# Kernel tuning notes

Measured on AMD Instinct MI355X. Metric: run time of the kernel, lower is better.

Reference implementation:

```python
import jax, jax.numpy as jnp
import numpy as np

D_MODEL = 1024
N_HEAD = 16
D_K = D_MODEL // N_HEAD


def setup_inputs() -> dict:
    key = jax.random.key(0)
    ks = jax.random.split(key, 11)
    B, S = 4, 2048
    s = 1.0 / np.sqrt(D_MODEL)
    return {
        "q": jax.random.normal(ks[0], (B, S, D_MODEL), jnp.float32),
        "k": jax.random.normal(ks[1], (B, S, D_MODEL), jnp.float32),
        "v": jax.random.normal(ks[2], (B, S, D_MODEL), jnp.float32),
        "w_q": jax.random.normal(ks[3], (D_MODEL, D_MODEL), jnp.float32) * s,
        "b_q": jnp.zeros((D_MODEL,), jnp.float32),
        "w_k": jax.random.normal(ks[4], (D_MODEL, D_MODEL), jnp.float32) * s,
        "b_k": jnp.zeros((D_MODEL,), jnp.float32),
        "w_v": jax.random.normal(ks[5], (D_MODEL, D_MODEL), jnp.float32) * s,
        "b_v": jnp.zeros((D_MODEL,), jnp.float32),
        "w_o": jax.random.normal(ks[6], (D_MODEL, D_MODEL), jnp.float32) * s,
        "b_o": jnp.zeros((D_MODEL,), jnp.float32),
    }


def reference(q, k, v, w_q, b_q, w_k, b_k, w_v, b_v, w_o, b_o):
    B, S, _ = q.shape
    # projections (torch Linear: x @ W^T + b)
    qp = q @ w_q.T + b_q
    kp = k @ w_k.T + b_k
    vp = v @ w_v.T + b_v
    # split heads -> [B, H, S, d_k]
    qh = qp.reshape(B, S, N_HEAD, D_K).transpose(0, 2, 1, 3)
    kh = kp.reshape(B, S, N_HEAD, D_K).transpose(0, 2, 1, 3)
    vh = vp.reshape(B, S, N_HEAD, D_K).transpose(0, 2, 1, 3)
    # scaled dot-product attention
    scores = jnp.einsum("bhqd,bhkd->bhqk", qh, kh) / jnp.sqrt(jnp.float32(D_K)).astype(qh.dtype)
    attn = jax.nn.softmax(scores, axis=-1)
    out = jnp.einsum("bhqk,bhkd->bhqd", attn, vh)
    # merge heads -> [B, S, d_model]
    out = out.transpose(0, 2, 1, 3).reshape(B, S, D_MODEL)
    return out @ w_o.T + b_o
```

## Files before the change

kernel.cpp:

```cpp
#include <hip/hip_runtime.h>
#include <hip/hip_bf16.h>
#include <stdint.h>

#define D_MODEL 1024
#define SEQ     2048
#define NBATCH  4
#define NHEAD   16
#define MROWS   (NBATCH*SEQ)

typedef __attribute__((ext_vector_type(8))) short short8;
typedef __attribute__((ext_vector_type(4))) float floatx4;
typedef __attribute__((ext_vector_type(2))) unsigned int uint2v;

#if __has_builtin(__builtin_amdgcn_exp2f)
#define EXP2(x) __builtin_amdgcn_exp2f(x)
#else
#define EXP2(x) exp2f(x)
#endif

__device__ __forceinline__ unsigned short f2bf(float f) {
  unsigned int x;
  __builtin_memcpy(&x, &f, 4);
  x += 0x7fffu + ((x >> 16) & 1u);
  return (unsigned short)(x >> 16);
}

__device__ __forceinline__ unsigned int pk2(float a, float b) {
  __hip_bfloat162 h = __float22bfloat162_rn(make_float2(a, b));
  unsigned int u;
  __builtin_memcpy(&u, &h, 4);
  return u;
}

__device__ __forceinline__ void gl_lds16(const unsigned short* g, unsigned short* l) {
  __builtin_amdgcn_global_load_lds(
      (const __attribute__((address_space(1))) unsigned int*)g,
      (__attribute__((address_space(3))) unsigned int*)l, 16, 0, 0);
}

__global__ __launch_bounds__(256)
void cvt_all(const float* __restrict__ q, const float* __restrict__ k,
             const float* __restrict__ v, const float* __restrict__ wq,
             const float* __restrict__ wk, const float* __restrict__ wv,
             const float* __restrict__ wo,
             unsigned short* __restrict__ dq, unsigned short* __restrict__ dk,
             unsigned short* __restrict__ dv, unsigned short* __restrict__ dwq,
             unsigned short* __restrict__ dwk, unsigned short* __restrict__ dwv,
             unsigned short* __restrict__ dwo) {
  const unsigned QV4 = (MROWS * D_MODEL) / 4u;
  const unsigned WV4 = (D_MODEL * D_MODEL) / 4u;
  const unsigned total = 3u * QV4 + 4u * WV4;
  for (unsigned i = blockIdx.x * 256u + threadIdx.x; i < total;
       i += gridDim.x * 256u) {
    const float* s;
    unsigned short* d;
    unsigned off;
    if (i < 3u * QV4) {
      const unsigned t = i >> 21;
      off = i & (QV4 - 1u);
      s = (t == 0) ? q : (t == 1) ? k : v;
      d = (t == 0) ? dq : (t == 1) ? dk : dv;
    } else {
      const unsigned j = i - 3u * QV4;
      const unsigned t = j >> 18;
      off = j & (WV4 - 1u);
      s = (t == 0) ? wq : (t == 1) ? wk : (t == 2) ? wv : wo;
      d = (t == 0) ? dwq : (t == 1) ? dwk : (t == 2) ? dwv : dwo;
    }
    const floatx4 f = *(const floatx4*)(s + (size_t)off * 4);
    uint2v u;
    u.x = pk2(f[0], f[1]);
    u.y = pk2(f[2], f[3]);
    *(uint2v*)(d + (size_t)off * 4) = u;
  }
}

template <bool OUT_F32>
__global__ __launch_bounds__(256)
void gemm_bt_bias(const unsigned short* __restrict__ A,
                  const unsigned short* __restrict__ W,
                  const float* __restrict__ bias, void* __restrict__ Y_,
                  int M, int N, int K, float scale) {
  __shared__ __attribute__((aligned(16))) unsigned short As[2][128 * 32];
  __shared__ __attribute__((aligned(16))) unsigned short Bs[2][128 * 32];
  const int tid  = threadIdx.x;
  const int lane = tid & 63;
  const int w    = tid >> 6;
  const int rho  = lane & 15;
  const int quad = lane >> 4;
  const int ntile = N >> 7;
  const int cpx = gridDim.x >> 3;
  const int wg  = (blockIdx.x & 7) * cpx + (blockIdx.x >> 3);
  const int bx = wg % ntile;
  const int by = wg / ntile;
  const int tm = by << 7, tn = bx << 7;
  const int wrow = (w >> 1) << 6;
  const int wcol = (w & 1) << 6;

  const int srow = lane >> 2;
  const int scol = (lane & 3) << 3;
  const unsigned short* gA = A + (size_t)(tm + w * 32 + srow) * K + scol;
  const unsigned short* gB = W + (size_t)(tn + w * 32 + srow) * K + scol;
  unsigned short* lA0 = &As[0][(w * 32) * 32];
  unsigned short* lA1 = &As[1][(w * 32) * 32];
  unsigned short* lB0 = &Bs[0][(w * 32) * 32];
  unsigned short* lB1 = &Bs[1][(w * 32) * 32];

  floatx4 acc[4][4] = {};

  gl_lds16(gA, lA0);
  gl_lds16(gA + 16 * (size_t)K, lA0 + 16 * 32);
  gl_lds16(gB, lB0);
  gl_lds16(gB + 16 * (size_t)K, lB0 + 16 * 32);
  __syncthreads();

  for (int kk = 0; kk < K; kk += 32) {
    const int cur = (kk >> 5) & 1;
    if (kk + 32 < K) {
      unsigned short* dA = cur ? lA0 : lA1;
      unsigned short* dB = cur ? lB0 : lB1;
      gl_lds16(gA + kk + 32, dA);
      gl_lds16(gA + 16 * (size_t)K + kk + 32, dA + 16 * 32);
      gl_lds16(gB + kk + 32, dB);
      gl_lds16(gB + 16 * (size_t)K + kk + 32, dB + 16 * 32);
    }
    const unsigned short* as = &As[cur][0];
    const unsigned short* bs = &Bs[cur][0];
    short8 af[4], bfr[4];
#pragma unroll
    for (int i = 0; i < 4; i++) {
      af[i]  = *(const short8*)&as[(wrow + i * 16 + rho) * 32 + quad * 8];
      bfr[i] = *(const short8*)&bs[(wcol + i * 16 + rho) * 32 + quad * 8];
    }
#pragma unroll
    for (int i = 0; i < 4; i++)
#pragma unroll
      for (int j = 0; j < 4; j++)
        acc[i][j] = __builtin_amdgcn_mfma_f32_16x16x32_bf16(af[i], bfr[j],
                                                            acc[i][j], 0, 0, 0);
    __syncthreads();
  }

  float bj[4];
#pragma unroll
  for (int j = 0; j < 4; j++) bj[j] = bias[tn + wcol + j * 16 + rho];
#pragma unroll
  for (int i = 0; i < 4; i++) {
    const int grow = tm + wrow + i * 16 + (quad << 2);
#pragma unroll
    for (int j = 0; j < 4; j++) {
      const int gcol = tn + wcol + j * 16 + rho;
#pragma unroll
      for (int r = 0; r < 4; r++) {
        const float val = (acc[i][j][r] + bj[j]) * scale;
        if (OUT_F32)
          ((float*)Y_)[(size_t)(grow + r) * N + gcol] = val;
        else
          ((unsigned short*)Y_)[(size_t)(grow + r) * N + gcol] = f2bf(val);
      }
    }
  }
}

__global__ __launch_bounds__(256, 3)
void attn_fused(const unsigned short* __restrict__ Qp,
                const unsigned short* __restrict__ Kp,
                const unsigned short* __restrict__ Vp,
                unsigned short* __restrict__ AO) {
  __shared__ unsigned short Ks[2][64*64];
  __shared__ unsigned short Vt[2][64*72];
  __shared__ unsigned short Pl[4][32*72];

  const int tid  = threadIdx.x;
  const int w    = tid >> 6;
  const int lane = tid & 63;
  const int rho  = lane & 15;
  const int quad = lane >> 4;

  const int qt = blockIdx.x & 15;
  const int bh = blockIdx.x >> 4;
  const int b  = bh >> 4;
  const int h  = bh & 15;
  const size_t base = (size_t)b*SEQ*D_MODEL + h*64;
  const unsigned short* Qb = Qp + base;
  const unsigned short* Kb = Kp + base;
  const unsigned short* Vb = Vp + base;

  const int q0 = qt*128 + w*32;

  short8 aq[2][2];
#pragma unroll
  for (int u = 0; u < 2; u++) {
    const unsigned short* qr = Qb + (size_t)(q0 + u*16 + rho)*D_MODEL + quad*8;
    aq[u][0] = *(const short8*)qr;
    aq[u][1] = *(const short8*)(qr + 32);
  }

  float lsum[2][4] = {};
  floatx4 oacc[2][4] = {};

  const int vkey = tid & 63;
  const int vh   = tid >> 6;
  const int vkap = ((vkey & 15) << 2) | (vkey >> 4);

  const int s0 = w*64 + lane;
  const int k0key = s0 >> 3, k0g = ((s0 & 7) - k0key) & 7;
  const int s1 = 256 + w*64 + lane;
  const int k1key = s1 >> 3, k1g = ((s1 & 7) - k1key) & 7;

  const int kp0 = (quad + rho) & 7;
  const int kp1 = (kp0 + 4) & 7;

  gl_lds16(Kb + (size_t)k0key*D_MODEL + k0g*8, &Ks[0][(w*64)*8]);
  gl_lds16(Kb + (size_t)k1key*D_MODEL + k1g*8, &Ks[0][(256 + w*64)*8]);

  for (int kb = 0; kb < SEQ; kb += 64) {
    const int bi = (kb >> 6) & 1;

    {
      const unsigned short* vr = Vb + (size_t)(kb + vkey)*D_MODEL + vh*16;
      const short8 v0 = *(const short8*)vr;
      const short8 v1 = *(const short8*)(vr + 8);
      unsigned short* dst = &Vt[bi][vh*16*72 + vkap];
#pragma unroll
      for (int e = 0; e < 8; e++) dst[e*72] = (unsigned short)v0[e];
#pragma unroll
      for (int e = 0; e < 8; e++) dst[(8 + e)*72] = (unsigned short)v1[e];
    }
    __syncthreads();

    if (kb + 64 < SEQ) {
      unsigned short* kn = &Ks[bi ^ 1][0];
      gl_lds16(Kb + (size_t)(kb + 64 + k0key)*D_MODEL + k0g*8, kn + (w*64)*8);
      gl_lds16(Kb + (size_t)(kb + 64 + k1key)*D_MODEL + k1g*8, kn + (256 + w*64)*8);
    }

    const unsigned short* ks = &Ks[bi][0];
    floatx4 s[2][4];
#pragma unroll
    for (int gk = 0; gk < 4; gk++) {
      const int key = gk*16 + rho;
      const short8 kf0 = *(const short8*)(ks + (key*8 + kp0)*8);
      const short8 kf1 = *(const short8*)(ks + (key*8 + kp1)*8);
#pragma unroll
      for (int u = 0; u < 2; u++) {
        floatx4 t = {0.f, 0.f, 0.f, 0.f};
        t = __builtin_amdgcn_mfma_f32_16x16x32_bf16(aq[u][0], kf0, t, 0, 0, 0);
        t = __builtin_amdgcn_mfma_f32_16x16x32_bf16(aq[u][1], kf1, t, 0, 0, 0);
        s[u][gk] = t;
      }
    }

#pragma unroll
    for (int u = 0; u < 2; u++)
#pragma unroll
      for (int r = 0; r < 4; r++) {
        const float e0 = EXP2(s[u][0][r]);
        const float e1 = EXP2(s[u][1][r]);
        const float e2 = EXP2(s[u][2][r]);
        const float e3 = EXP2(s[u][3][r]);
        lsum[u][r] += (e0 + e1) + (e2 + e3);
        const unsigned int lo = pk2(e0, e1);
        const unsigned int hi = pk2(e2, e3);
        const int row = u*16 + (quad << 2) + r;
        *(uint2v*)&Pl[w][row*72 + rho*4] = (uint2v){lo, hi};
      }

    short8 bv[4][2];
#pragma unroll
    for (int c = 0; c < 4; c++) {
      bv[c][0] = *(const short8*)&Vt[bi][(c*16 + rho)*72 + quad*8];
      bv[c][1] = *(const short8*)&Vt[bi][(c*16 + rho)*72 + 32 + quad*8];
    }
#pragma unroll
    for (int u = 0; u < 2; u++) {
      const short8 ap0 = *(const short8*)&Pl[w][(u*16 + rho)*72 + quad*8];
      const short8 ap1 = *(const short8*)&Pl[w][(u*16 + rho)*72 + 32 + quad*8];
#pragma unroll
      for (int c = 0; c < 4; c++) {
        oacc[u][c] = __builtin_amdgcn_mfma_f32_16x16x32_bf16(ap0, bv[c][0], oacc[u][c], 0, 0, 0);
        oacc[u][c] = __builtin_amdgcn_mfma_f32_16x16x32_bf16(ap1, bv[c][1], oacc[u][c], 0, 0, 0);
      }
    }
  }

#pragma unroll
  for (int d = 1; d < 16; d <<= 1)
#pragma unroll
    for (int u = 0; u < 2; u++)
#pragma unroll
      for (int r = 0; r < 4; r++) lsum[u][r] += __shfl_xor(lsum[u][r], d);

#pragma unroll
  for (int u = 0; u < 2; u++) {
    float inv[4];
#pragma unroll
    for (int r = 0; r < 4; r++) inv[r] = 1.0f / lsum[u][r];
#pragma unroll
    for (int c = 0; c < 4; c++)
#pragma unroll
      for (int r = 0; r < 4; r++)
        AO[base + (size_t)(q0 + u*16 + (quad << 2) + r)*D_MODEL + c*16 + rho] =
            f2bf(oacc[u][c][r] * inv[r]);
  }
}

extern "C" void kernel_launch(void* const* d_in, const int* in_sizes, int n_in,
                              void* d_out, int out_size, void* d_ws, size_t ws_size,
                              hipStream_t stream) {
  const float* q  = (const float*)d_in[0];
  const float* k  = (const float*)d_in[1];
  const float* v  = (const float*)d_in[2];
  const float* wq = (const float*)d_in[3];
  const float* bq = (const float*)d_in[4];
  const float* wk = (const float*)d_in[5];
  const float* bk = (const float*)d_in[6];
  const float* wv = (const float*)d_in[7];
  const float* bv = (const float*)d_in[8];
  const float* wo = (const float*)d_in[9];
  const float* bo = (const float*)d_in[10];
  float* out = (float*)d_out;

  unsigned short* Qp  = (unsigned short*)d_ws;
  unsigned short* Kp  = Qp + (size_t)MROWS*D_MODEL;
  unsigned short* Vp  = Kp + (size_t)MROWS*D_MODEL;
  unsigned short* AO  = Vp + (size_t)MROWS*D_MODEL;
  unsigned short* qb  = AO + (size_t)MROWS*D_MODEL;
  unsigned short* kb  = qb + (size_t)MROWS*D_MODEL;
  unsigned short* vb  = kb + (size_t)MROWS*D_MODEL;
  unsigned short* wqb = vb + (size_t)MROWS*D_MODEL;
  unsigned short* wkb = wqb + (size_t)D_MODEL*D_MODEL;
  unsigned short* wvb = wkb + (size_t)D_MODEL*D_MODEL;
  unsigned short* wob = wvb + (size_t)D_MODEL*D_MODEL;

  const float qscale = 0.125f * 1.4426950408889634f;

  const dim3 blk(256);
  cvt_all<<<dim3(2048), blk, 0, stream>>>(q, k, v, wq, wk, wv, wo,
                                          qb, kb, vb, wqb, wkb, wvb, wob);

  const dim3 ggrid((D_MODEL/128) * (MROWS/128));
  gemm_bt_bias<false><<<ggrid, blk, 0, stream>>>(qb, wqb, bq, Qp, MROWS, D_MODEL, D_MODEL, qscale);
  gemm_bt_bias<false><<<ggrid, blk, 0, stream>>>(kb, wkb, bk, Kp, MROWS, D_MODEL, D_MODEL, 1.0f);
  gemm_bt_bias<false><<<ggrid, blk, 0, stream>>>(vb, wvb, bv, Vp, MROWS, D_MODEL, D_MODEL, 1.0f);
  attn_fused<<<dim3(NBATCH*NHEAD*(SEQ/128)), blk, 0, stream>>>(Qp, Kp, Vp, AO);
  gemm_bt_bias<true><<<ggrid, blk, 0, stream>>>(AO, wob, bo, out, MROWS, D_MODEL, D_MODEL, 1.0f);
}
```

Baseline: 382.3 us.

## Batch QKV GEMMs, deepen GEMM K-tile, and double attention rows per warp

The three QKV projection GEMMs become one launch that uses a grid y-dimension to pick the matrix. The GEMM K-step grows from 32 to 64 with a rotated LDS layout to avoid bank conflicts, and occupancy is lowered to 2 blocks. Attention now gives each warp 64 query rows instead of 32, so every K/V tile staged in LDS is reused across twice as many rows. The aim is to cut launch overhead, barrier count and K/V reload traffic, in exchange for higher register and LDS use and fewer, larger attention blocks.

```diff
diff --git a/kernel.cpp b/kernel.cpp
--- a/kernel.cpp
+++ b/kernel.cpp
@@ -75,14 +75,13 @@
   }
 }
 
-template <bool OUT_F32>
-__global__ __launch_bounds__(256)
-void gemm_bt_bias(const unsigned short* __restrict__ A,
-                  const unsigned short* __restrict__ W,
-                  const float* __restrict__ bias, void* __restrict__ Y_,
-                  int M, int N, int K, float scale) {
-  __shared__ __attribute__((aligned(16))) unsigned short As[2][128 * 32];
-  __shared__ __attribute__((aligned(16))) unsigned short Bs[2][128 * 32];
+template <int OMODE>
+__device__ __forceinline__ void gemm_body(const unsigned short* __restrict__ A,
+                                          const unsigned short* __restrict__ W,
+                                          const float* __restrict__ bias,
+                                          void* __restrict__ Y_,
+                                          int M, int N, int K, float scale,
+                                          unsigned short* As, unsigned short* Bs) {
   const int tid  = threadIdx.x;
   const int lane = tid & 63;
   const int w    = tid >> 6;
@@ -97,49 +96,47 @@
   const int wrow = (w >> 1) << 6;
   const int wcol = (w & 1) << 6;
 
-  const int srow = lane >> 2;
-  const int scol = (lane & 3) << 3;
-  const unsigned short* gA = A + (size_t)(tm + w * 32 + srow) * K + scol;
-  const unsigned short* gB = W + (size_t)(tn + w * 32 + srow) * K + scol;
-  unsigned short* lA0 = &As[0][(w * 32) * 32];
-  unsigned short* lA1 = &As[1][(w * 32) * 32];
-  unsigned short* lB0 = &Bs[0][(w * 32) * 32];
-  unsigned short* lB1 = &Bs[1][(w * 32) * 32];
+  const int lrow = lane >> 3;
+  const int g    = ((lane & 7) - lrow) & 7;
+  const unsigned short* gA = A + (size_t)(tm + w * 32 + lrow) * K + g * 8;
+  const unsigned short* gB = W + (size_t)(tn + w * 32 + lrow) * K + g * 8;
 
   floatx4 acc[4][4] = {};
 
-  gl_lds16(gA, lA0);
-  gl_lds16(gA + 16 * (size_t)K, lA0 + 16 * 32);
-  gl_lds16(gB, lB0);
-  gl_lds16(gB + 16 * (size_t)K, lB0 + 16 * 32);
+#define GSTAGE(buf, kk)                                                        \
+  _Pragma("unroll") for (int c = 0; c < 4; c++) {                              \
+    gl_lds16(gA + (size_t)c * 8 * K + (kk), &As[(buf)*8192 + (w*256 + c*64)*8]); \
+    gl_lds16(gB + (size_t)c * 8 * K + (kk), &Bs[(buf)*8192 + (w*256 + c*64)*8]); \
+  }
+
+  GSTAGE(0, 0);
   __syncthreads();
 
-  for (int kk = 0; kk < K; kk += 32) {
-    const int cur = (kk >> 5) & 1;
-    if (kk + 32 < K) {
-      unsigned short* dA = cur ? lA0 : lA1;
-      unsigned short* dB = cur ? lB0 : lB1;
-      gl_lds16(gA + kk + 32, dA);
-      gl_lds16(gA + 16 * (size_t)K + kk + 32, dA + 16 * 32);
-      gl_lds16(gB + kk + 32, dB);
-      gl_lds16(gB + 16 * (size_t)K + kk + 32, dB + 16 * 32);
-    }
-    const unsigned short* as = &As[cur][0];
-    const unsigned short* bs = &Bs[cur][0];
-    short8 af[4], bfr[4];
-#pragma unroll
-    for (int i = 0; i < 4; i++) {
-      af[i]  = *(const short8*)&as[(wrow + i * 16 + rho) * 32 + quad * 8];
-      bfr[i] = *(const short8*)&bs[(wcol + i * 16 + rho) * 32 + quad * 8];
-    }
-#pragma unroll
-    for (int i = 0; i < 4; i++)
+  for (int kk = 0; kk < K; kk += 64) {
+    const int cur = (kk >> 6) & 1;
+    if (kk + 64 < K) { GSTAGE(cur ^ 1, kk + 64); }
+    const unsigned short* as = &As[cur * 8192];
+    const unsigned short* bs = &Bs[cur * 8192];
+#pragma unroll
+    for (int h = 0; h < 2; h++) {
+      const int kp = (quad + rho + h * 4) & 7;
+      short8 af[4], bf4[4];
+#pragma unroll
+      for (int i = 0; i < 4; i++)
+        af[i] = *(const short8*)&as[(wrow + i * 16 + rho) * 64 + kp * 8];
 #pragma unroll
       for (int j = 0; j < 4; j++)
-        acc[i][j] = __builtin_amdgcn_mfma_f32_16x16x32_bf16(af[i], bfr[j],
-                                                            acc[i][j], 0, 0, 0);
+        bf4[j] = *(const short8*)&bs[(wcol + j * 16 + rho) * 64 + kp * 8];
+#pragma unroll
+      for (int i = 0; i < 4; i++)
+#pragma unroll
+        for (int j = 0; j < 4; j++)
+          acc[i][j] = __builtin_amdgcn_mfma_f32_16x16x32_bf16(af[i], bf4[j],
+                                                              acc[i][j], 0, 0, 0);
+    }
     __syncthreads();
   }
+#undef GSTAGE
 
   float bj[4];
 #pragma unroll
@@ -153,7 +150,7 @@
 #pragma unroll
       for (int r = 0; r < 4; r++) {
         const float val = (acc[i][j][r] + bj[j]) * scale;
-        if (OUT_F32)
+        if (OMODE == 1)
           ((float*)Y_)[(size_t)(grow + r) * N + gcol] = val;
         else
           ((unsigned short*)Y_)[(size_t)(grow + r) * N + gcol] = f2bf(val);
@@ -162,14 +159,44 @@
   }
 }
 
-__global__ __launch_bounds__(256, 3)
+template <int OMODE>
+__global__ __launch_bounds__(256, 2)
+void gemm_one(const unsigned short* __restrict__ A,
+              const unsigned short* __restrict__ W,
+              const float* __restrict__ bias, void* __restrict__ Y_,
+              int M, int N, int K, float scale) {
+  __shared__ __attribute__((aligned(16))) unsigned short As[2 * 128 * 64];
+  __shared__ __attribute__((aligned(16))) unsigned short Bs[2 * 128 * 64];
+  gemm_body<OMODE>(A, W, bias, Y_, M, N, K, scale, As, Bs);
+}
+
+__global__ __launch_bounds__(256, 2)
+void gemm_qkv(const unsigned short* __restrict__ qb, const unsigned short* __restrict__ wqb,
+              const float* __restrict__ bq, unsigned short* __restrict__ Qp,
+              const unsigned short* __restrict__ kb, const unsigned short* __restrict__ wkb,
+              const float* __restrict__ bk, unsigned short* __restrict__ Kp,
+              const unsigned short* __restrict__ vb, const unsigned short* __restrict__ wvb,
+              const float* __restrict__ bv, unsigned short* __restrict__ Vp,
+              float qscale) {
+  __shared__ __attribute__((aligned(16))) unsigned short As[2 * 128 * 64];
+  __shared__ __attribute__((aligned(16))) unsigned short Bs[2 * 128 * 64];
+  const int y = blockIdx.y;
+  const unsigned short* A = (y == 0) ? qb : (y == 1) ? kb : vb;
+  const unsigned short* W = (y == 0) ? wqb : (y == 1) ? wkb : wvb;
+  const float* bias       = (y == 0) ? bq : (y == 1) ? bk : bv;
+  unsigned short* Y       = (y == 0) ? Qp : (y == 1) ? Kp : Vp;
+  const float scale = (y == 0) ? qscale : 1.0f;
+  gemm_body<0>(A, W, bias, Y, MROWS, D_MODEL, D_MODEL, scale, As, Bs);
+}
+
+__global__ __launch_bounds__(256, 2)
 void attn_fused(const unsigned short* __restrict__ Qp,
                 const unsigned short* __restrict__ Kp,
                 const unsigned short* __restrict__ Vp,
                 unsigned short* __restrict__ AO) {
   __shared__ unsigned short Ks[2][64*64];
   __shared__ unsigned short Vt[2][64*72];
-  __shared__ unsigned short Pl[4][32*72];
+  __shared__ unsigned short Pl[4][64*72];
 
   const int tid  = threadIdx.x;
   const int w    = tid >> 6;
@@ -177,8 +204,8 @@
   const int rho  = lane & 15;
   const int quad = lane >> 4;
 
-  const int qt = blockIdx.x & 15;
-  const int bh = blockIdx.x >> 4;
+  const int qt = blockIdx.x & 7;
+  const int bh = blockIdx.x >> 3;
   const int b  = bh >> 4;
   const int h  = bh & 15;
   const size_t base = (size_t)b*SEQ*D_MODEL + h*64;
@@ -186,21 +213,20 @@
   const unsigned short* Kb = Kp + base;
   const unsigned short* Vb = Vp + base;
 
-  const int q0 = qt*128 + w*32;
-
-  short8 aq[2][2];
-#pragma unroll
-  for (int u = 0; u < 2; u++) {
+  const int q0 = qt*256 + w*64;
+
+  short8 aq[4][2];
+#pragma unroll
+  for (int u = 0; u < 4; u++) {
     const unsigned short* qr = Qb + (size_t)(q0 + u*16 + rho)*D_MODEL + quad*8;
     aq[u][0] = *(const short8*)qr;
     aq[u][1] = *(const short8*)(qr + 32);
   }
 
-  float lsum[2][4] = {};
-  floatx4 oacc[2][4] = {};
-
-  const int vkey = tid & 63;
-  const int vh   = tid >> 6;
+  float lsum[4][4] = {};
+  floatx4 oacc[4][4] = {};
+
+  const int vkey = lane;
   const int vkap = ((vkey & 15) << 2) | (vkey >> 4);
 
   const int s0 = w*64 + lane;
@@ -218,10 +244,10 @@
     const int bi = (kb >> 6) & 1;
 
     {
-      const unsigned short* vr = Vb + (size_t)(kb + vkey)*D_MODEL + vh*16;
+      const unsigned short* vr = Vb + (size_t)(kb + vkey)*D_MODEL + w*16;
       const short8 v0 = *(const short8*)vr;
       const short8 v1 = *(const short8*)(vr + 8);
-      unsigned short* dst = &Vt[bi][vh*16*72 + vkap];
+      unsigned short* dst = &Vt[bi][w*16*72 + vkap];
 #pragma unroll
       for (int e = 0; e < 8; e++) dst[e*72] = (unsigned short)v0[e];
 #pragma unroll
@@ -236,29 +262,29 @@
     }
 
     const unsigned short* ks = &Ks[bi][0];
-    floatx4 s[2][4];
+    floatx4 sc[4][4];
 #pragma unroll
     for (int gk = 0; gk < 4; gk++) {
       const int key = gk*16 + rho;
       const short8 kf0 = *(const short8*)(ks + (key*8 + kp0)*8);
       const short8 kf1 = *(const short8*)(ks + (key*8 + kp1)*8);
 #pragma unroll
-      for (int u = 0; u < 2; u++) {
+      for (int u = 0; u < 4; u++) {
         floatx4 t = {0.f, 0.f, 0.f, 0.f};
         t = __builtin_amdgcn_mfma_f32_16x16x32_bf16(aq[u][0], kf0, t, 0, 0, 0);
         t = __builtin_amdgcn_mfma_f32_16x16x32_bf16(aq[u][1], kf1, t, 0, 0, 0);
-        s[u][gk] = t;
+        sc[u][gk] = t;
       }
     }
 
 #pragma unroll
-    for (int u = 0; u < 2; u++)
+    for (int u = 0; u < 4; u++)
 #pragma unroll
       for (int r = 0; r < 4; r++) {
-        const float e0 = EXP2(s[u][0][r]);
-        const float e1 = EXP2(s[u][1][r]);
-        const float e2 = EXP2(s[u][2][r]);
-        const float e3 = EXP2(s[u][3][r]);
+        const float e0 = EXP2(sc[u][0][r]);
+        const float e1 = EXP2(sc[u][1][r]);
+        const float e2 = EXP2(sc[u][2][r]);
+        const float e3 = EXP2(sc[u][3][r]);
         lsum[u][r] += (e0 + e1) + (e2 + e3);
         const unsigned int lo = pk2(e0, e1);
         const unsigned int hi = pk2(e2, e3);
@@ -273,7 +299,7 @@
       bv[c][1] = *(const short8*)&Vt[bi][(c*16 + rho)*72 + 32 + quad*8];
     }
 #pragma unroll
-    for (int u = 0; u < 2; u++) {
+    for (int u = 0; u < 4; u++) {
       const short8 ap0 = *(const short8*)&Pl[w][(u*16 + rho)*72 + quad*8];
       const short8 ap1 = *(const short8*)&Pl[w][(u*16 + rho)*72 + 32 + quad*8];
 #pragma unroll
@@ -287,12 +313,12 @@
 #pragma unroll
   for (int d = 1; d < 16; d <<= 1)
 #pragma unroll
-    for (int u = 0; u < 2; u++)
+    for (int u = 0; u < 4; u++)
 #pragma unroll
       for (int r = 0; r < 4; r++) lsum[u][r] += __shfl_xor(lsum[u][r], d);
 
 #pragma unroll
-  for (int u = 0; u < 2; u++) {
+  for (int u = 0; u < 4; u++) {
     float inv[4];
 #pragma unroll
     for (int r = 0; r < 4; r++) inv[r] = 1.0f / lsum[u][r];
@@ -339,10 +365,11 @@
   cvt_all<<<dim3(2048), blk, 0, stream>>>(q, k, v, wq, wk, wv, wo,
                                           qb, kb, vb, wqb, wkb, wvb, wob);
 
-  const dim3 ggrid((D_MODEL/128) * (MROWS/128));
-  gemm_bt_bias<false><<<ggrid, blk, 0, stream>>>(qb, wqb, bq, Qp, MROWS, D_MODEL, D_MODEL, qscale);
-  gemm_bt_bias<false><<<ggrid, blk, 0, stream>>>(kb, wkb, bk, Kp, MROWS, D_MODEL, D_MODEL, 1.0f);
-  gemm_bt_bias<false><<<ggrid, blk, 0, stream>>>(vb, wvb, bv, Vp, MROWS, D_MODEL, D_MODEL, 1.0f);
-  attn_fused<<<dim3(NBATCH*NHEAD*(SEQ/128)), blk, 0, stream>>>(Qp, Kp, Vp, AO);
-  gemm_bt_bias<true><<<ggrid, blk, 0, stream>>>(AO, wob, bo, out, MROWS, D_MODEL, D_MODEL, 1.0f);
-}
+  gemm_qkv<<<dim3((D_MODEL/128) * (MROWS/128), 3), blk, 0, stream>>>(
+      qb, wqb, bq, Qp, kb, wkb, bk, Kp, vb, wvb, bv, Vp, qscale);
+
+  attn_fused<<<dim3(NBATCH*NHEAD*(SEQ/256)), blk, 0, stream>>>(Qp, Kp, Vp, AO);
+
+  gemm_one<1><<<dim3((D_MODEL/128) * (MROWS/128)), blk, 0, stream>>>(
+      AO, wob, bo, out, MROWS, D_MODEL, D_MODEL, 1.0f);
+}
```

After: 337.7 us. -11.6%, faster.
